# Kernel tuning notes

Measured on AMD Instinct MI355X. Metric: run time of the kernel, lower is better.

The kernel has to match this reference:

```python
import jax, jax.numpy as jnp
import numpy as np

N0, N1, N2 = 400000, 100000, 20000   # source nodes per sampled layer; dst nodes are a prefix
E1, E2 = 1000000, 200000
IN, HID, HEADS, OUT = 128, 256, 4, 47
C = HID // HEADS
EPS = 1e-5
NEG_SLOPE = 0.2


def setup_inputs() -> dict:
    key = jax.random.key(0)
    ks = jax.random.split(key, 20)
    def rn(i, shape, s=0.1):
        return jax.random.normal(ks[i], shape, jnp.float32) * s
    inp = {}
    inp["x"] = jax.random.normal(ks[0], (N0, IN), jnp.float32)
    inp["src1"] = jax.random.randint(ks[1], (E1,), 0, N0, jnp.int32)
    inp["dst1"] = jax.random.randint(ks[2], (E1,), 0, N1, jnp.int32)
    inp["src2"] = jax.random.randint(ks[3], (E2,), 0, N1, jnp.int32)
    inp["dst2"] = jax.random.randint(ks[4], (E2,), 0, N2, jnp.int32)
    # layer 1 GAT + skip + BN
    inp["W1"] = rn(5, (IN, HID)); inp["a_src1"] = rn(6, (HEADS, C)); inp["a_dst1"] = rn(7, (HEADS, C))
    inp["b1"] = jnp.zeros((HID,), jnp.float32)
    inp["Wsk1"] = rn(8, (IN, HID)); inp["bsk1"] = jnp.zeros((HID,), jnp.float32)
    inp["g1"] = jnp.ones((HID,), jnp.float32); inp["be1"] = jnp.zeros((HID,), jnp.float32)
    # layer 2 GAT + skip + BN
    inp["W2"] = rn(9, (HID, HID)); inp["a_src2"] = rn(10, (HEADS, C)); inp["a_dst2"] = rn(11, (HEADS, C))
    inp["b2"] = jnp.zeros((HID,), jnp.float32)
    inp["Wsk2"] = rn(12, (HID, HID)); inp["bsk2"] = jnp.zeros((HID,), jnp.float32)
    inp["g2"] = jnp.ones((HID,), jnp.float32); inp["be2"] = jnp.zeros((HID,), jnp.float32)
    # MLP head
    inp["Wm1"] = rn(13, (HID, HID)); inp["bm1"] = jnp.zeros((HID,), jnp.float32)
    inp["gm"] = jnp.ones((HID,), jnp.float32); inp["bem"] = jnp.zeros((HID,), jnp.float32)
    inp["Wm2"] = rn(14, (HID, OUT)); inp["bm2"] = jnp.zeros((OUT,), jnp.float32)
    return inp


def batch_norm(x, gamma, beta):
    mu = jnp.mean(x, axis=0)
    var = jnp.mean(jnp.square(x - mu), axis=0)  # biased var, as torch BN training
    return (x - mu) * jax.lax.rsqrt(var + EPS) * gamma + beta


def edge_softmax(logits, dst, n_dst):
    # logits: [E, H]; softmax over incoming edges per destination node
    m = jax.ops.segment_max(logits, dst, num_segments=n_dst)
    m = jax.lax.stop_gradient(jnp.where(jnp.isfinite(m), m, 0.0))
    e = jnp.exp(logits - m[dst])
    s = jax.ops.segment_sum(e, dst, num_segments=n_dst)
    return e / (s[dst] + 1e-16)


def gat_layer(x, n_dst, src, dst, W, a_src, a_dst, b, Wsk, bsk, gamma, beta):
    # GATConv (PyG, shared src/dst linear since in_channels is int) on bipartite (x, x[:n_dst])
    xp = (x @ W).reshape(-1, HEADS, C)                       # [N, H, C]
    al_s = jnp.einsum('nhc,hc->nh', xp, a_src)               # [N, H]
    al_d = jnp.einsum('nhc,hc->nh', xp[:n_dst], a_dst)       # [n_dst, H]
    logits = jax.nn.leaky_relu(al_s[src] + al_d[dst], NEG_SLOPE)   # [E, H]
    alpha = edge_softmax(logits, dst, n_dst)                 # [E, H]
    msg = xp[src] * alpha[:, :, None]                        # [E, H, C]
    out = jax.ops.segment_sum(msg, dst, num_segments=n_dst).reshape(n_dst, HID) + b
    out = out + x[:n_dst] @ Wsk + bsk                        # skip connection
    return jax.nn.elu(batch_norm(out, gamma, beta))          # dropout omitted (eval)


def reference(x, src1, dst1, src2, dst2,
              W1, a_src1, a_dst1, b1, Wsk1, bsk1, g1, be1,
              W2, a_src2, a_dst2, b2, Wsk2, bsk2, g2, be2,
              Wm1, bm1, gm, bem, Wm2, bm2):
    h = gat_layer(x, N1, src1, dst1, W1, a_src1, a_dst1, b1, Wsk1, bsk1, g1, be1)
    h = gat_layer(h, N2, src2, dst2, W2, a_src2, a_dst2, b2, Wsk2, bsk2, g2, be2)
    # MLP head: Linear -> BN -> ReLU -> (Dropout) -> Linear
    h = jax.nn.relu(batch_norm(h @ Wm1 + bm1, gm, bem))
    return h @ Wm2 + bm2                                     # logits [N2, OUT]
```

## Files before the change

kernel.cpp:

```cpp
#include <hip/hip_runtime.h>
#include <math.h>

constexpr int kN0 = 400000, kN1 = 100000, kN2 = 20000;
constexpr int kE1 = 1000000, kE2 = 200000;
constexpr int kIN = 128, kHID = 256, kOUT = 47;
constexpr float kEPS = 1e-5f, kNEG = 0.2f;

#define DEV static __device__ __forceinline__

typedef __attribute__((ext_vector_type(8))) short short8;
typedef __attribute__((ext_vector_type(4))) float f32x4;

DEV float b2f(unsigned short u) { return __uint_as_float(((unsigned)u) << 16); }
DEV unsigned short f2bf(float f) {
    unsigned u = __float_as_uint(f);
    unsigned r = (u + 0x7fffu + ((u >> 16) & 1u)) >> 16;
    return (unsigned short)r;
}
DEV float lrelu(float v) { return v > 0.f ? v : kNEG * v; }

DEV void gload_lds16(const void* g, void* l) {
    __builtin_amdgcn_global_load_lds(
        (const __attribute__((address_space(1))) void*)g,
        (__attribute__((address_space(3))) void*)l, 16, 0, 0);
}

constexpr int kNZreg = 1536 + 2 * kN1 + 2 * kN2;
__global__ void prep_all(const float* __restrict__ W1, const float* __restrict__ as1,
                         const float* __restrict__ ad1,
                         const float* __restrict__ W2, const float* __restrict__ as2,
                         const float* __restrict__ ad2,
                         const float* __restrict__ Wsk1, const float* __restrict__ Wsk2,
                         const float* __restrict__ Wm1,
                         float* __restrict__ zreg,
                         unsigned short* __restrict__ v1t, unsigned short* __restrict__ v2t,
                         unsigned short* __restrict__ Wcat1t,
                         unsigned short* __restrict__ Wcat2t,
                         unsigned short* __restrict__ Wm1t) {
    int i = blockIdx.x * blockDim.x + threadIdx.x;
    if (i < kNZreg) { zreg[i] = 0.f; return; }
    i -= kNZreg;
    if (i < 2048) {
        int j = i >> 7, k = i & 127;
        float s = 0.f;
        if (j < 8) {
            int h = j & 3;
            const float* a = (j >= 4) ? ad1 : as1;
            for (int c = 0; c < 64; ++c) s += W1[(size_t)k * 256 + h * 64 + c] * a[h * 64 + c];
        }
        v1t[i] = f2bf(s);
        return;
    }
    i -= 2048;
    if (i < 4096) {
        int j = i >> 8, k = i & 255;
        float s = 0.f;
        if (j < 8) {
            int h = j & 3;
            const float* a = (j >= 4) ? ad2 : as2;
            for (int c = 0; c < 64; ++c) s += W2[(size_t)k * 256 + h * 64 + c] * a[h * 64 + c];
        }
        v2t[i] = f2bf(s);
        return;
    }
    i -= 4096;
    if (i < 163840) {
        int n = i / 640, k = i % 640;
        float v;
        if (k < 512) { int h = k >> 7, kin = k & 127; v = ((n >> 6) == h) ? W1[(size_t)kin * 256 + n] : 0.f; }
        else v = Wsk1[(size_t)(k - 512) * 256 + n];
        Wcat1t[i] = f2bf(v);
        return;
    }
    i -= 163840;
    if (i < 327680) {
        int n = i / 1280, k = i % 1280;
        float v;
        if (k < 1024) { int h = k >> 8, kin = k & 255; v = ((n >> 6) == h) ? W2[(size_t)kin * 256 + n] : 0.f; }
        else v = Wsk2[(size_t)(k - 1024) * 256 + n];
        Wcat2t[i] = f2bf(v);
        return;
    }
    i -= 327680;
    if (i < 65536) {
        int n = i >> 8, k = i & 255;
        Wm1t[i] = f2bf(Wm1[(size_t)k * 256 + n]);
    }
}

__global__ __launch_bounds__(256) void conv_als_mfma(const float* __restrict__ x,
                                                     const unsigned short* __restrict__ v1t,
                                                     unsigned short* __restrict__ xb,
                                                     float* __restrict__ als,
                                                     float* __restrict__ ald) {
    int wid = threadIdx.x >> 6, lane = threadIdx.x & 63;
    int l15 = lane & 15, l4 = lane >> 4;
    short8 bfr[4];
    #pragma unroll
    for (int ks = 0; ks < 4; ++ks)
        bfr[ks] = *reinterpret_cast<const short8*>(&v1t[l15 * 128 + ks * 32 + l4 * 8]);

    const int ntile = kN0 / 16;
    int nw = gridDim.x * 4;
    for (int t = blockIdx.x * 4 + wid; t < ntile; t += nw) {
        int base = t * 16;
        int r = base + l15;
        f32x4 acc = (f32x4){0.f, 0.f, 0.f, 0.f};
        #pragma unroll
        for (int ks = 0; ks < 4; ++ks) {
            size_t o = (size_t)r * 128 + ks * 32 + l4 * 8;
            float4 xa = *reinterpret_cast<const float4*>(&x[o]);
            float4 xc = *reinterpret_cast<const float4*>(&x[o + 4]);
            short8 af;
            af[0] = (short)f2bf(xa.x); af[1] = (short)f2bf(xa.y);
            af[2] = (short)f2bf(xa.z); af[3] = (short)f2bf(xa.w);
            af[4] = (short)f2bf(xc.x); af[5] = (short)f2bf(xc.y);
            af[6] = (short)f2bf(xc.z); af[7] = (short)f2bf(xc.w);
            *reinterpret_cast<short8*>(&xb[o]) = af;
            acc = __builtin_amdgcn_mfma_f32_16x16x32_bf16(af, bfr[ks], acc, 0, 0, 0);
        }
        if (l15 < 8) {
            #pragma unroll
            for (int i = 0; i < 4; ++i) {
                int node = base + l4 * 4 + i;
                if (l15 < 4) als[(size_t)node * 4 + l15] = acc[i];
                else if (node < kN1) ald[(size_t)node * 4 + (l15 - 4)] = acc[i];
            }
        }
    }
}

template <bool AL>
__global__ __launch_bounds__(256) void bn_mfma(const unsigned short* __restrict__ X,
                                               const float* __restrict__ stats,
                                               const float* __restrict__ gamma,
                                               const float* __restrict__ beta,
                                               unsigned short* __restrict__ outb,
                                               const unsigned short* __restrict__ v2t,
                                               float* __restrict__ als,
                                               float* __restrict__ ald,
                                               int M, int Ndst) {
    __shared__ float smu[256], ssc[256], ssh[256];
    {
        int c = threadIdx.x;
        float invM = 1.f / (float)M;
        float mu = stats[c] * invM;
        float var = stats[256 + c] * invM - mu * mu;
        smu[c] = mu;
        ssc[c] = rsqrtf(var + kEPS) * gamma[c];
        ssh[c] = beta[c];
    }
    __syncthreads();

    int wid = threadIdx.x >> 6, lane = threadIdx.x & 63;
    int l15 = lane & 15, l4 = lane >> 4;
    short8 bfr[8];
    if (AL) {
        #pragma unroll
        for (int ks = 0; ks < 8; ++ks)
            bfr[ks] = *reinterpret_cast<const short8*>(&v2t[l15 * 256 + ks * 32 + l4 * 8]);
    }

    const int ntile = M / 16;
    int nw = gridDim.x * 4;
    for (int t = blockIdx.x * 4 + wid; t < ntile; t += nw) {
        int base = t * 16;
        int r = base + l15;
        f32x4 acc = (f32x4){0.f, 0.f, 0.f, 0.f};
        #pragma unroll
        for (int ks = 0; ks < 8; ++ks) {
            int c0 = ks * 32 + l4 * 8;
            size_t o = (size_t)r * 256 + c0;
            short8 xr = *reinterpret_cast<const short8*>(&X[o]);
            float4 mua = *reinterpret_cast<const float4*>(&smu[c0]);
            float4 muc = *reinterpret_cast<const float4*>(&smu[c0 + 4]);
            float4 sca = *reinterpret_cast<const float4*>(&ssc[c0]);
            float4 scc = *reinterpret_cast<const float4*>(&ssc[c0 + 4]);
            float4 sha = *reinterpret_cast<const float4*>(&ssh[c0]);
            float4 shc = *reinterpret_cast<const float4*>(&ssh[c0 + 4]);
            float v[8];
            v[0] = (b2f((unsigned short)xr[0]) - mua.x) * sca.x + sha.x;
            v[1] = (b2f((unsigned short)xr[1]) - mua.y) * sca.y + sha.y;
            v[2] = (b2f((unsigned short)xr[2]) - mua.z) * sca.z + sha.z;
            v[3] = (b2f((unsigned short)xr[3]) - mua.w) * sca.w + sha.w;
            v[4] = (b2f((unsigned short)xr[4]) - muc.x) * scc.x + shc.x;
            v[5] = (b2f((unsigned short)xr[5]) - muc.y) * scc.y + shc.y;
            v[6] = (b2f((unsigned short)xr[6]) - muc.z) * scc.z + shc.z;
            v[7] = (b2f((unsigned short)xr[7]) - muc.w) * scc.w + shc.w;
            short8 af;
            #pragma unroll
            for (int i = 0; i < 8; ++i) {
                float tv = v[i] > 0.f ? v[i] : expm1f(v[i]);
                af[i] = (short)f2bf(tv);
            }
            *reinterpret_cast<short8*>(&outb[o]) = af;
            if (AL) acc = __builtin_amdgcn_mfma_f32_16x16x32_bf16(af, bfr[ks], acc, 0, 0, 0);
        }
        if (AL && l15 < 8) {
            #pragma unroll
            for (int i = 0; i < 4; ++i) {
                int node = base + l4 * 4 + i;
                if (l15 < 4) als[(size_t)node * 4 + l15] = acc[i];
                else if (node < Ndst) ald[(size_t)node * 4 + (l15 - 4)] = acc[i];
            }
        }
    }
}

__global__ void hist_both(const int* __restrict__ dst1, int* __restrict__ cnt1, int E1,
                          const int* __restrict__ dst2, int* __restrict__ cnt2, int E2) {
    int e = blockIdx.x * blockDim.x + threadIdx.x;
    if (e < E1) atomicAdd(&cnt1[dst1[e]], 1);
    else if (e - E1 < E2) atomicAdd(&cnt2[dst2[e - E1]], 1);
}

__global__ __launch_bounds__(256) void scan_block_both(const int* __restrict__ cnt1, int n1,
                                                       int* __restrict__ offs1, int* __restrict__ bsum1, int nb1,
                                                       const int* __restrict__ cnt2, int n2,
                                                       int* __restrict__ offs2, int* __restrict__ bsum2) {
    const int* counts; int n; int* offs; int* bsum; int b;
    if ((int)blockIdx.x < nb1) { counts = cnt1; n = n1; offs = offs1; bsum = bsum1; b = blockIdx.x; }
    else { counts = cnt2; n = n2; offs = offs2; bsum = bsum2; b = blockIdx.x - nb1; }
    __shared__ int sh[256];
    int tid = threadIdx.x;
    int base = b * 1024 + tid * 4;
    int c0 = (base + 0 < n) ? counts[base + 0] : 0;
    int c1 = (base + 1 < n) ? counts[base + 1] : 0;
    int c2 = (base + 2 < n) ? counts[base + 2] : 0;
    int c3 = (base + 3 < n) ? counts[base + 3] : 0;
    int tot = c0 + c1 + c2 + c3;
    sh[tid] = tot;
    __syncthreads();
    for (int o = 1; o < 256; o <<= 1) {
        int t = (tid >= o) ? sh[tid - o] : 0;
        __syncthreads();
        sh[tid] += t;
        __syncthreads();
    }
    int excl = sh[tid] - tot;
    if (base + 0 < n) offs[base + 0] = excl;
    if (base + 1 < n) offs[base + 1] = excl + c0;
    if (base + 2 < n) offs[base + 2] = excl + c0 + c1;
    if (base + 3 < n) offs[base + 3] = excl + c0 + c1 + c2;
    if (tid == 255) bsum[b] = sh[255];
}

__global__ __launch_bounds__(256) void scan_bsums_both(const int* __restrict__ bsum1,
                                                       int* __restrict__ bscan1, int nb1,
                                                       const int* __restrict__ bsum2,
                                                       int* __restrict__ bscan2, int nb2) {
    __shared__ int sh[256];
    int tid = threadIdx.x;
    int v = (tid < nb1) ? bsum1[tid] : 0;
    sh[tid] = v;
    __syncthreads();
    for (int o = 1; o < 256; o <<= 1) {
        int t = (tid >= o) ? sh[tid - o] : 0;
        __syncthreads();
        sh[tid] += t;
        __syncthreads();
    }
    if (tid < nb1) bscan1[tid] = sh[tid] - v;
    __syncthreads();
    int v2 = (tid < nb2) ? bsum2[tid] : 0;
    sh[tid] = v2;
    __syncthreads();
    for (int o = 1; o < 256; o <<= 1) {
        int t = (tid >= o) ? sh[tid - o] : 0;
        __syncthreads();
        sh[tid] += t;
        __syncthreads();
    }
    if (tid < nb2) bscan2[tid] = sh[tid] - v2;
}

__global__ void scan_add_both(int* __restrict__ offs1, const int* __restrict__ bscan1,
                              const int* __restrict__ cnt1, int n1,
                              int* __restrict__ offs2, const int* __restrict__ bscan2,
                              const int* __restrict__ cnt2, int n2) {
    int i = blockIdx.x * blockDim.x + threadIdx.x;
    if (i < n1) {
        int v = offs1[i] + bscan1[i >> 10];
        offs1[i] = v;
        if (i == n1 - 1) offs1[n1] = v + cnt1[i];
    } else {
        int j = i - n1;
        if (j < n2) {
            int v = offs2[j] + bscan2[j >> 10];
            offs2[j] = v;
            if (j == n2 - 1) offs2[n2] = v + cnt2[j];
        }
    }
}

__global__ void csr_scatter_w(const int* __restrict__ dst, const int* __restrict__ src,
                              const int* __restrict__ offs,
                              const float* __restrict__ als, const float* __restrict__ ald,
                              int* __restrict__ cur, int* __restrict__ srcs,
                              float4* __restrict__ wbuf, int E) {
    int e = blockIdx.x * blockDim.x + threadIdx.x;
    if (e >= E) return;
    int d = dst[e], s = src[e];
    int pos = offs[d] + atomicAdd(&cur[d], 1);
    srcs[pos] = s;
    float4 a = *reinterpret_cast<const float4*>(&als[(size_t)s * 4]);
    float4 b = *reinterpret_cast<const float4*>(&ald[(size_t)d * 4]);
    float4 w;
    w.x = expf(lrelu(a.x + b.x));
    w.y = expf(lrelu(a.y + b.y));
    w.z = expf(lrelu(a.z + b.z));
    w.w = expf(lrelu(a.w + b.w));
    wbuf[pos] = w;
}

template <bool OUTBF, bool STATS>
__global__ __launch_bounds__(512) void gemm_pipe(const unsigned short* __restrict__ A1, int K1,
                                                 const unsigned short* __restrict__ A2, int K2,
                                                 const unsigned short* __restrict__ Bt,
                                                 void* __restrict__ Cv,
                                                 const float* __restrict__ bias1,
                                                 const float* __restrict__ bias2,
                                                 float* __restrict__ stats,
                                                 int M, int N, int rs, int kwin) {
    __shared__ unsigned short SH[4][128 * 64];
    const int tid = threadIdx.x;
    const int wid = tid >> 6, lane = tid & 63;
    const int wr = wid >> 2, wc = wid & 3;
    const int l15 = lane & 15, l4 = lane >> 4;
    const int m0 = blockIdx.y * 128, n0 = blockIdx.x * 128;
    const int rsub = lane >> 3;
    const int kslot = (lane & 7) ^ rsub;
    const int KB = K1 + K2;
    const int nwin = kwin >> 6;
    const int nt = nwin + (K2 >> 6);
    const int wbase = n0 * rs;

    auto stage = [&](int buf, int t) {
        const unsigned short* Asrc; int ka, lda, gk;
        if (t < nwin) { gk = wbase + (t << 6); Asrc = A1; ka = gk; lda = K1; }
        else { int t2 = t - nwin; gk = K1 + (t2 << 6); Asrc = A2; ka = t2 << 6; lda = K2; }
        #pragma unroll
        for (int c = 0; c < 2; ++c) {
            int q = wid * 2 + c;
            int rowA = m0 + q * 8 + rsub; if (rowA > M - 1) rowA = M - 1;
            gload_lds16(Asrc + (size_t)rowA * lda + ka + kslot * 8, &SH[buf][q * 512]);
            int rowB = n0 + q * 8 + rsub;
            gload_lds16(Bt + (size_t)rowB * KB + gk + kslot * 8, &SH[2 + buf][q * 512]);
        }
    };

    f32x4 acc[4][2];
    #pragma unroll
    for (int i = 0; i < 4; ++i)
        #pragma unroll
        for (int j = 0; j < 2; ++j) acc[i][j] = (f32x4){0.f, 0.f, 0.f, 0.f};

    stage(0, 0);
    __syncthreads();
    for (int t = 0; t < nt; ++t) {
        if (t + 1 < nt) stage((t + 1) & 1, t + 1);
        int b = t & 1;
        short8 af[2][4], bf[2][2];
        #pragma unroll
        for (int kk = 0; kk < 2; ++kk) {
            #pragma unroll
            for (int mi = 0; mi < 4; ++mi) {
                int row = wr * 64 + mi * 16 + l15;
                af[kk][mi] = *reinterpret_cast<const short8*>(
                    &SH[b][row * 64 + (((kk * 4 + l4) ^ (row & 7)) << 3)]);
            }
            #pragma unroll
            for (int ni = 0; ni < 2; ++ni) {
                int row = wc * 32 + ni * 16 + l15;
                bf[kk][ni] = *reinterpret_cast<const short8*>(
                    &SH[2 + b][row * 64 + (((kk * 4 + l4) ^ (row & 7)) << 3)]);
            }
        }
        #pragma unroll
        for (int kk = 0; kk < 2; ++kk)
            #pragma unroll
            for (int mi = 0; mi < 4; ++mi)
                #pragma unroll
                for (int ni = 0; ni < 2; ++ni)
                    acc[mi][ni] = __builtin_amdgcn_mfma_f32_16x16x32_bf16(
                        af[kk][mi], bf[kk][ni], acc[mi][ni], 0, 0, 0);
        __syncthreads();
    }

    float csum[2] = {0.f, 0.f}, csq[2] = {0.f, 0.f};
    unsigned short* LB = (unsigned short*)SH;
    float* LF = (float*)SH;
    #pragma unroll
    for (int mi = 0; mi < 4; ++mi) {
        int lrow0 = wr * 64 + mi * 16 + l4 * 4;
        #pragma unroll
        for (int ni = 0; ni < 2; ++ni) {
            int lcol = wc * 32 + ni * 16 + l15;
            int col = n0 + lcol;
            float badd = 0.f;
            if (bias1) badd += bias1[col];
            if (bias2) badd += bias2[col];
            f32x4 v = acc[mi][ni];
            #pragma unroll
            for (int i = 0; i < 4; ++i) {
                float o = v[i] + badd;
                if (STATS && (m0 + lrow0 + i) < M) { csum[ni] += o; csq[ni] += o * o; }
                if (OUTBF) LB[(lrow0 + i) * 128 + lcol] = f2bf(o);
                else LF[(lrow0 + i) * 128 + lcol] = o;
            }
        }
    }
    if (STATS) {
        #pragma unroll
        for (int ni = 0; ni < 2; ++ni) {
            float s = csum[ni], q = csq[ni];
            s += __shfl_xor(s, 16, 64); q += __shfl_xor(q, 16, 64);
            s += __shfl_xor(s, 32, 64); q += __shfl_xor(q, 32, 64);
            if (l4 == 0) {
                int col = n0 + wc * 32 + ni * 16 + l15;
                atomicAdd(&stats[col], s);
                atomicAdd(&stats[256 + col], q);
            }
        }
    }
    __syncthreads();
    if (OUTBF) {
        unsigned short* Cb = (unsigned short*)Cv;
        #pragma unroll
        for (int it = 0; it < 4; ++it) {
            int lin = (it * 512 + tid) * 8;
            int r = lin >> 7, c0 = lin & 127;
            int gr = m0 + r;
            if (gr < M)
                *reinterpret_cast<short8*>(&Cb[(size_t)gr * N + n0 + c0]) =
                    *reinterpret_cast<const short8*>(&LB[lin]);
        }
    } else {
        float* Cf = (float*)Cv;
        #pragma unroll
        for (int it = 0; it < 8; ++it) {
            int lin = (it * 512 + tid) * 4;
            int r = lin >> 7, c0 = lin & 127;
            int gr = m0 + r;
            if (gr < M)
                *reinterpret_cast<float4*>(&Cf[(size_t)gr * N + n0 + c0]) =
                    *reinterpret_cast<const float4*>(&LF[lin]);
        }
    }
}

__global__ __launch_bounds__(256) void fused_agg1(const unsigned short* __restrict__ xb,
                                                  const float4* __restrict__ wbuf,
                                                  const int* __restrict__ srcs,
                                                  const int* __restrict__ offs,
                                                  unsigned short* __restrict__ Agg, int Ndst) {
    int d = blockIdx.x * 4 + (threadIdx.x >> 6);
    if (d >= Ndst) return;
    int lane = threadIdx.x & 63;
    int beg = offs[d], end = offs[d + 1];
    float ac[4][2] = {};
    float se0 = 0.f, se1 = 0.f, se2 = 0.f, se3 = 0.f;

    auto edge = [&](int i) {
        int s = srcs[i];
        float4 w = wbuf[i];
        unsigned xv = *reinterpret_cast<const unsigned*>(&xb[(size_t)s * 128 + lane * 2]);
        se0 += w.x; se1 += w.y; se2 += w.z; se3 += w.w;
        float fx = b2f((unsigned short)(xv & 0xffff));
        float fy = b2f((unsigned short)(xv >> 16));
        ac[0][0] = fmaf(w.x, fx, ac[0][0]); ac[0][1] = fmaf(w.x, fy, ac[0][1]);
        ac[1][0] = fmaf(w.y, fx, ac[1][0]); ac[1][1] = fmaf(w.y, fy, ac[1][1]);
        ac[2][0] = fmaf(w.z, fx, ac[2][0]); ac[2][1] = fmaf(w.z, fy, ac[2][1]);
        ac[3][0] = fmaf(w.w, fx, ac[3][0]); ac[3][1] = fmaf(w.w, fy, ac[3][1]);
    };
    int i = beg;
    for (; i + 4 <= end; i += 4) { edge(i); edge(i + 1); edge(i + 2); edge(i + 3); }
    for (; i < end; ++i) edge(i);

    float inv0 = 1.f / (se0 + 1e-16f), inv1 = 1.f / (se1 + 1e-16f);
    float inv2 = 1.f / (se2 + 1e-16f), inv3 = 1.f / (se3 + 1e-16f);
    unsigned short* row = Agg + (size_t)d * 512;
    ushort2 o;
    o.x = f2bf(ac[0][0] * inv0); o.y = f2bf(ac[0][1] * inv0);
    *reinterpret_cast<ushort2*>(&row[0 * 128 + lane * 2]) = o;
    o.x = f2bf(ac[1][0] * inv1); o.y = f2bf(ac[1][1] * inv1);
    *reinterpret_cast<ushort2*>(&row[1 * 128 + lane * 2]) = o;
    o.x = f2bf(ac[2][0] * inv2); o.y = f2bf(ac[2][1] * inv2);
    *reinterpret_cast<ushort2*>(&row[2 * 128 + lane * 2]) = o;
    o.x = f2bf(ac[3][0] * inv3); o.y = f2bf(ac[3][1] * inv3);
    *reinterpret_cast<ushort2*>(&row[3 * 128 + lane * 2]) = o;
}

__global__ __launch_bounds__(256) void fused_agg2(const unsigned short* __restrict__ hb,
                                                  const float4* __restrict__ wbuf,
                                                  const int* __restrict__ srcs,
                                                  const int* __restrict__ offs,
                                                  unsigned short* __restrict__ Agg, int Ndst) {
    int d = blockIdx.x * 4 + (threadIdx.x >> 6);
    if (d >= Ndst) return;
    int lane = threadIdx.x & 63;
    int beg = offs[d], end = offs[d + 1];
    float ac[4][4] = {};
    float se0 = 0.f, se1 = 0.f, se2 = 0.f, se3 = 0.f;

    auto edge = [&](int i) {
        int s = srcs[i];
        float4 w = wbuf[i];
        ushort4 xv = *reinterpret_cast<const ushort4*>(&hb[(size_t)s * 256 + lane * 4]);
        se0 += w.x; se1 += w.y; se2 += w.z; se3 += w.w;
        float f0 = b2f(xv.x), f1 = b2f(xv.y), f2 = b2f(xv.z), f3 = b2f(xv.w);
        ac[0][0] = fmaf(w.x, f0, ac[0][0]); ac[0][1] = fmaf(w.x, f1, ac[0][1]);
        ac[0][2] = fmaf(w.x, f2, ac[0][2]); ac[0][3] = fmaf(w.x, f3, ac[0][3]);
        ac[1][0] = fmaf(w.y, f0, ac[1][0]); ac[1][1] = fmaf(w.y, f1, ac[1][1]);
        ac[1][2] = fmaf(w.y, f2, ac[1][2]); ac[1][3] = fmaf(w.y, f3, ac[1][3]);
        ac[2][0] = fmaf(w.z, f0, ac[2][0]); ac[2][1] = fmaf(w.z, f1, ac[2][1]);
        ac[2][2] = fmaf(w.z, f2, ac[2][2]); ac[2][3] = fmaf(w.z, f3, ac[2][3]);
        ac[3][0] = fmaf(w.w, f0, ac[3][0]); ac[3][1] = fmaf(w.w, f1, ac[3][1]);
        ac[3][2] = fmaf(w.w, f2, ac[3][2]); ac[3][3] = fmaf(w.w, f3, ac[3][3]);
    };
    int i = beg;
    for (; i + 2 <= end; i += 2) { edge(i); edge(i + 1); }
    for (; i < end; ++i) edge(i);

    float inv[4] = {1.f / (se0 + 1e-16f), 1.f / (se1 + 1e-16f),
                    1.f / (se2 + 1e-16f), 1.f / (se3 + 1e-16f)};
    unsigned short* row = Agg + (size_t)d * 1024;
    #pragma unroll
    for (int h = 0; h < 4; ++h) {
        ushort4 o;
        o.x = f2bf(ac[h][0] * inv[h]); o.y = f2bf(ac[h][1] * inv[h]);
        o.z = f2bf(ac[h][2] * inv[h]); o.w = f2bf(ac[h][3] * inv[h]);
        *reinterpret_cast<ushort4*>(&row[h * 256 + lane * 4]) = o;
    }
}

__global__ __launch_bounds__(256) void gemm64_bn(const unsigned short* __restrict__ A,
                                                 const float* __restrict__ B,
                                                 float* __restrict__ Cmat,
                                                 const float* __restrict__ bias,
                                                 const float* __restrict__ stats,
                                                 const float* __restrict__ gamma,
                                                 const float* __restrict__ beta,
                                                 int M, int N, int K) {
    __shared__ float As[32][68];
    __shared__ float Bs[32][68];
    __shared__ float bnsc[256], bnsh[256];
    const int tid = threadIdx.x;
    {
        int c = tid;
        float invM = 1.f / (float)M;
        float mu = stats[c] * invM;
        float var = stats[256 + c] * invM - mu * mu;
        float sc = rsqrtf(var + kEPS) * gamma[c];
        bnsc[c] = sc;
        bnsh[c] = beta[c] - mu * sc;
    }
    __syncthreads();
    const int tx = tid & 15, ty = tid >> 4;
    const int m0 = blockIdx.y * 64, n0 = blockIdx.x * 64;
    float acc[4][4] = {};

    for (int k0 = 0; k0 < K; k0 += 32) {
        #pragma unroll
        for (int t = 0; t < 2; ++t) {
            int i = tid + t * 256;
            int row = i >> 3;
            int kq = (i & 7) << 2;
            ushort4 u = make_ushort4(0, 0, 0, 0);
            int gr = m0 + row;
            if (gr < M) u = *reinterpret_cast<const ushort4*>(&A[(size_t)gr * K + k0 + kq]);
            #pragma unroll
            for (int j = 0; j < 4; ++j) {
                int k = k0 + kq + j;
                unsigned short uv = (j == 0) ? u.x : (j == 1) ? u.y : (j == 2) ? u.z : u.w;
                float v = b2f(uv) * bnsc[k] + bnsh[k];
                As[kq + j][row] = fmaxf(v, 0.f);
            }
        }
        #pragma unroll
        for (int t = 0; t < 2; ++t) {
            int i = tid + t * 256;
            int kr = i >> 4;
            int cq = (i & 15) << 2;
            #pragma unroll
            for (int j = 0; j < 4; ++j) {
                int gc = n0 + cq + j;
                Bs[kr][cq + j] = (gc < N) ? B[(size_t)(k0 + kr) * N + gc] : 0.f;
            }
        }
        __syncthreads();
        #pragma unroll
        for (int kk = 0; kk < 32; ++kk) {
            float4 a4 = *reinterpret_cast<const float4*>(&As[kk][ty << 2]);
            float4 b4 = *reinterpret_cast<const float4*>(&Bs[kk][tx << 2]);
            float a[4] = {a4.x, a4.y, a4.z, a4.w};
            float b[4] = {b4.x, b4.y, b4.z, b4.w};
            #pragma unroll
            for (int i2 = 0; i2 < 4; ++i2)
                #pragma unroll
                for (int j = 0; j < 4; ++j)
                    acc[i2][j] = fmaf(a[i2], b[j], acc[i2][j]);
        }
        __syncthreads();
    }

    #pragma unroll
    for (int i2 = 0; i2 < 4; ++i2) {
        int row = m0 + (ty << 2) + i2;
        if (row >= M) continue;
        #pragma unroll
        for (int j = 0; j < 4; ++j) {
            int col = n0 + (tx << 2) + j;
            if (col >= N) continue;
            Cmat[(size_t)row * N + col] = acc[i2][j] + bias[col];
        }
    }
}

extern "C" void kernel_launch(void* const* d_in, const int* in_sizes, int n_in,
                              void* d_out, int out_size, void* d_ws, size_t ws_size,
                              hipStream_t stream) {
    (void)in_sizes; (void)n_in; (void)out_size; (void)ws_size;

    const float* x      = (const float*)d_in[0];
    const int*   src1   = (const int*)d_in[1];
    const int*   dst1   = (const int*)d_in[2];
    const int*   src2   = (const int*)d_in[3];
    const int*   dst2   = (const int*)d_in[4];
    const float* W1     = (const float*)d_in[5];
    const float* a_src1 = (const float*)d_in[6];
    const float* a_dst1 = (const float*)d_in[7];
    const float* b1     = (const float*)d_in[8];
    const float* Wsk1   = (const float*)d_in[9];
    const float* bsk1   = (const float*)d_in[10];
    const float* g1     = (const float*)d_in[11];
    const float* be1    = (const float*)d_in[12];
    const float* W2     = (const float*)d_in[13];
    const float* a_src2 = (const float*)d_in[14];
    const float* a_dst2 = (const float*)d_in[15];
    const float* b2     = (const float*)d_in[16];
    const float* Wsk2   = (const float*)d_in[17];
    const float* bsk2   = (const float*)d_in[18];
    const float* g2     = (const float*)d_in[19];
    const float* be2    = (const float*)d_in[20];
    const float* Wm1    = (const float*)d_in[21];
    const float* bm1    = (const float*)d_in[22];
    const float* gm     = (const float*)d_in[23];
    const float* bem    = (const float*)d_in[24];
    const float* Wm2    = (const float*)d_in[25];
    const float* bm2    = (const float*)d_in[26];

    float* ws = (float*)d_ws;
    size_t off = 0;
    auto alloc = [&](size_t n) { float* p = ws + off; off += n; return p; };
    unsigned short* xb    = (unsigned short*)alloc((size_t)kN0 * 128 / 2);
    unsigned short* Agg1  = (unsigned short*)alloc((size_t)kN1 * 512 / 2);
    unsigned short* Agg2  = (unsigned short*)alloc((size_t)kN2 * 1024 / 2);
    unsigned short* h1pre = (unsigned short*)alloc((size_t)kN1 * 256 / 2);
    unsigned short* h1b   = (unsigned short*)alloc((size_t)kN1 * 256 / 2);
    unsigned short* h2pre = (unsigned short*)alloc((size_t)kN2 * 256 / 2);
    unsigned short* h2b   = (unsigned short*)alloc((size_t)kN2 * 256 / 2);
    unsigned short* h3pre = (unsigned short*)alloc((size_t)kN2 * 256 / 2);
    unsigned short* Wcat1t = (unsigned short*)alloc(256 * 640 / 2);
    unsigned short* Wcat2t = (unsigned short*)alloc(256 * 1280 / 2);
    unsigned short* Wm1t   = (unsigned short*)alloc(256 * 256 / 2);
    unsigned short* v1t    = (unsigned short*)alloc(16 * 128 / 2);
    unsigned short* v2t    = (unsigned short*)alloc(16 * 256 / 2);
    float4* w1buf = (float4*)alloc((size_t)kE1 * 4);
    float4* w2buf = (float4*)alloc((size_t)kE2 * 4);
    float* als1 = alloc((size_t)kN0 * 4);
    float* ald1 = alloc((size_t)kN1 * 4);
    float* als2 = alloc((size_t)kN1 * 4);
    float* ald2 = alloc((size_t)kN2 * 4);
    float* zreg = alloc(kNZreg);
    float* stats1 = zreg, *stats2 = zreg + 512, *stats3 = zreg + 1024;
    int* cnt1 = (int*)(zreg + 1536);
    int* cur1 = cnt1 + kN1;
    int* cnt2 = cur1 + kN1;
    int* cur2 = cnt2 + kN2;
    int* srcs1  = (int*)alloc(kE1);
    int* offs1  = (int*)alloc(kN1 + 4);
    int* bsum1  = (int*)alloc(128);
    int* bscan1 = (int*)alloc(128);
    int* srcs2  = (int*)alloc(kE2);
    int* offs2  = (int*)alloc(kN2 + 4);
    int* bsum2  = (int*)alloc(128);
    int* bscan2 = (int*)alloc(128);

    hipStream_t st = stream;
    const int nb1 = (kN1 + 1023) / 1024;
    const int nb2 = (kN2 + 1023) / 1024;

    prep_all<<<(kNZreg + 563200 + 255) / 256, 256, 0, st>>>(
        W1, a_src1, a_dst1, W2, a_src2, a_dst2, Wsk1, Wsk2, Wm1,
        zreg, v1t, v2t, Wcat1t, Wcat2t, Wm1t);

    conv_als_mfma<<<2048, 256, 0, st>>>(x, v1t, xb, als1, ald1);

    hist_both<<<(kE1 + kE2 + 255) / 256, 256, 0, st>>>(dst1, cnt1, kE1, dst2, cnt2, kE2);
    scan_block_both<<<nb1 + nb2, 256, 0, st>>>(cnt1, kN1, offs1, bsum1, nb1, cnt2, kN2, offs2, bsum2);
    scan_bsums_both<<<1, 256, 0, st>>>(bsum1, bscan1, nb1, bsum2, bscan2, nb2);
    scan_add_both<<<(kN1 + kN2 + 255) / 256, 256, 0, st>>>(offs1, bscan1, cnt1, kN1,
                                                           offs2, bscan2, cnt2, kN2);
    csr_scatter_w<<<(kE1 + 255) / 256, 256, 0, st>>>(dst1, src1, offs1, als1, ald1,
                                                     cur1, srcs1, w1buf, kE1);

    fused_agg1<<<(kN1 + 3) / 4, 256, 0, st>>>(xb, w1buf, srcs1, offs1, Agg1, kN1);
    gemm_pipe<true, true><<<dim3(2, (kN1 + 127) / 128), 512, 0, st>>>(
        Agg1, 512, xb, 128, Wcat1t, h1pre, b1, bsk1, stats1, kN1, 256, 2, 256);
    bn_mfma<true><<<1024, 256, 0, st>>>(h1pre, stats1, g1, be1, h1b, v2t, als2, ald2, kN1, kN2);

    csr_scatter_w<<<(kE2 + 255) / 256, 256, 0, st>>>(dst2, src2, offs2, als2, ald2,
                                                     cur2, srcs2, w2buf, kE2);
    fused_agg2<<<(kN2 + 3) / 4, 256, 0, st>>>(h1b, w2buf, srcs2, offs2, Agg2, kN2);
    gemm_pipe<true, true><<<dim3(2, (kN2 + 127) / 128), 512, 0, st>>>(
        Agg2, 1024, h1b, 256, Wcat2t, h2pre, b2, bsk2, stats2, kN2, 256, 4, 512);
    bn_mfma<false><<<1024, 256, 0, st>>>(h2pre, stats2, g2, be2, h2b, nullptr, nullptr, nullptr,
                                         kN2, 0);

    gemm_pipe<true, true><<<dim3(2, (kN2 + 127) / 128), 512, 0, st>>>(
        h2b, 256, nullptr, 0, Wm1t, h3pre, bm1, nullptr, stats3, kN2, 256, 0, 256);
    gemm64_bn<<<dim3(1, (kN2 + 63) / 64), 256, 0, st>>>(
        h3pre, Wm2, (float*)d_out, bm2, stats3, gm, bem, kN2, kOUT, 256);
}
```

Measured before the change: 542.2 us.

## Fuse histogram into conv kernel, merge scan passes, batch aggregation loads

Measured after the change: 522.6 us. -3.6%, faster.

```diff
diff --git a/kernel.cpp b/kernel.cpp
--- a/kernel.cpp
+++ b/kernel.cpp
@@ -88,11 +88,22 @@
     }
 }
 
-__global__ __launch_bounds__(256) void conv_als_mfma(const float* __restrict__ x,
+constexpr int kConvBlocks = 2048;
+__global__ __launch_bounds__(256) void conv_als_hist(const float* __restrict__ x,
                                                      const unsigned short* __restrict__ v1t,
                                                      unsigned short* __restrict__ xb,
                                                      float* __restrict__ als,
-                                                     float* __restrict__ ald) {
+                                                     float* __restrict__ ald,
+                                                     const int* __restrict__ dst1,
+                                                     int* __restrict__ cnt1,
+                                                     const int* __restrict__ dst2,
+                                                     int* __restrict__ cnt2) {
+    if ((int)blockIdx.x >= kConvBlocks) {
+        int e = ((int)blockIdx.x - kConvBlocks) * 256 + threadIdx.x;
+        if (e < kE1) atomicAdd(&cnt1[dst1[e]], 1);
+        else { e -= kE1; if (e < kE2) atomicAdd(&cnt2[dst2[e]], 1); }
+        return;
+    }
     int wid = threadIdx.x >> 6, lane = threadIdx.x & 63;
     int l15 = lane & 15, l4 = lane >> 4;
     short8 bfr[4];
@@ -101,7 +112,7 @@
         bfr[ks] = *reinterpret_cast<const short8*>(&v1t[l15 * 128 + ks * 32 + l4 * 8]);
 
     const int ntile = kN0 / 16;
-    int nw = gridDim.x * 4;
+    const int nw = kConvBlocks * 4;
     for (int t = blockIdx.x * 4 + wid; t < ntile; t += nw) {
         int base = t * 16;
         int r = base + l15;
@@ -205,13 +216,6 @@
             }
         }
     }
-}
-
-__global__ void hist_both(const int* __restrict__ dst1, int* __restrict__ cnt1, int E1,
-                          const int* __restrict__ dst2, int* __restrict__ cnt2, int E2) {
-    int e = blockIdx.x * blockDim.x + threadIdx.x;
-    if (e < E1) atomicAdd(&cnt1[dst1[e]], 1);
-    else if (e - E1 < E2) atomicAdd(&cnt2[dst2[e - E1]], 1);
 }
 
 __global__ __launch_bounds__(256) void scan_block_both(const int* __restrict__ cnt1, int n1,
@@ -245,48 +249,29 @@
     if (tid == 255) bsum[b] = sh[255];
 }
 
-__global__ __launch_bounds__(256) void scan_bsums_both(const int* __restrict__ bsum1,
-                                                       int* __restrict__ bscan1, int nb1,
-                                                       const int* __restrict__ bsum2,
-                                                       int* __restrict__ bscan2, int nb2) {
-    __shared__ int sh[256];
-    int tid = threadIdx.x;
-    int v = (tid < nb1) ? bsum1[tid] : 0;
-    sh[tid] = v;
+__global__ __launch_bounds__(256) void scan_add_both(int* __restrict__ offs1,
+                                                     const int* __restrict__ bsum1,
+                                                     const int* __restrict__ cnt1, int n1, int nb1,
+                                                     int* __restrict__ offs2,
+                                                     const int* __restrict__ bsum2,
+                                                     const int* __restrict__ cnt2, int n2, int nb2) {
+    __shared__ int sb1[128], sb2[32];
+    if (threadIdx.x == 0) {
+        int acc = 0;
+        for (int j = 0; j < nb1; ++j) { sb1[j] = acc; acc += bsum1[j]; }
+        acc = 0;
+        for (int j = 0; j < nb2; ++j) { sb2[j] = acc; acc += bsum2[j]; }
+    }
     __syncthreads();
-    for (int o = 1; o < 256; o <<= 1) {
-        int t = (tid >= o) ? sh[tid - o] : 0;
-        __syncthreads();
-        sh[tid] += t;
-        __syncthreads();
-    }
-    if (tid < nb1) bscan1[tid] = sh[tid] - v;
-    __syncthreads();
-    int v2 = (tid < nb2) ? bsum2[tid] : 0;
-    sh[tid] = v2;
-    __syncthreads();
-    for (int o = 1; o < 256; o <<= 1) {
-        int t = (tid >= o) ? sh[tid - o] : 0;
-        __syncthreads();
-        sh[tid] += t;
-        __syncthreads();
-    }
-    if (tid < nb2) bscan2[tid] = sh[tid] - v2;
-}
-
-__global__ void scan_add_both(int* __restrict__ offs1, const int* __restrict__ bscan1,
-                              const int* __restrict__ cnt1, int n1,
-                              int* __restrict__ offs2, const int* __restrict__ bscan2,
-                              const int* __restrict__ cnt2, int n2) {
     int i = blockIdx.x * blockDim.x + threadIdx.x;
     if (i < n1) {
-        int v = offs1[i] + bscan1[i >> 10];
+        int v = offs1[i] + sb1[i >> 10];
         offs1[i] = v;
         if (i == n1 - 1) offs1[n1] = v + cnt1[i];
     } else {
         int j = i - n1;
         if (j < n2) {
-            int v = offs2[j] + bscan2[j >> 10];
+            int v = offs2[j] + sb2[j >> 10];
             offs2[j] = v;
             if (j == n2 - 1) offs2[n2] = v + cnt2[j];
         }
@@ -461,21 +446,29 @@
     float ac[4][2] = {};
     float se0 = 0.f, se1 = 0.f, se2 = 0.f, se3 = 0.f;
 
-    auto edge = [&](int i) {
-        int s = srcs[i];
-        float4 w = wbuf[i];
-        unsigned xv = *reinterpret_cast<const unsigned*>(&xb[(size_t)s * 128 + lane * 2]);
-        se0 += w.x; se1 += w.y; se2 += w.z; se3 += w.w;
-        float fx = b2f((unsigned short)(xv & 0xffff));
-        float fy = b2f((unsigned short)(xv >> 16));
-        ac[0][0] = fmaf(w.x, fx, ac[0][0]); ac[0][1] = fmaf(w.x, fy, ac[0][1]);
-        ac[1][0] = fmaf(w.y, fx, ac[1][0]); ac[1][1] = fmaf(w.y, fy, ac[1][1]);
-        ac[2][0] = fmaf(w.z, fx, ac[2][0]); ac[2][1] = fmaf(w.z, fy, ac[2][1]);
-        ac[3][0] = fmaf(w.w, fx, ac[3][0]); ac[3][1] = fmaf(w.w, fy, ac[3][1]);
-    };
-    int i = beg;
-    for (; i + 4 <= end; i += 4) { edge(i); edge(i + 1); edge(i + 2); edge(i + 3); }
-    for (; i < end; ++i) edge(i);
+    for (int i = beg; i < end; i += 4) {
+        int s[4]; float4 w[4]; unsigned xv[4];
+        #pragma unroll
+        for (int j = 0; j < 4; ++j) {
+            int idx = i + j < end ? i + j : end - 1;
+            s[j] = srcs[idx];
+            if (i + j < end) w[j] = wbuf[idx];
+            else w[j] = make_float4(0.f, 0.f, 0.f, 0.f);
+        }
+        #pragma unroll
+        for (int j = 0; j < 4; ++j)
+            xv[j] = *reinterpret_cast<const unsigned*>(&xb[(size_t)s[j] * 128 + lane * 2]);
+        #pragma unroll
+        for (int j = 0; j < 4; ++j) {
+            se0 += w[j].x; se1 += w[j].y; se2 += w[j].z; se3 += w[j].w;
+            float fx = b2f((unsigned short)(xv[j] & 0xffff));
+            float fy = b2f((unsigned short)(xv[j] >> 16));
+            ac[0][0] = fmaf(w[j].x, fx, ac[0][0]); ac[0][1] = fmaf(w[j].x, fy, ac[0][1]);
+            ac[1][0] = fmaf(w[j].y, fx, ac[1][0]); ac[1][1] = fmaf(w[j].y, fy, ac[1][1]);
+            ac[2][0] = fmaf(w[j].z, fx, ac[2][0]); ac[2][1] = fmaf(w[j].z, fy, ac[2][1]);
+            ac[3][0] = fmaf(w[j].w, fx, ac[3][0]); ac[3][1] = fmaf(w[j].w, fy, ac[3][1]);
+        }
+    }
 
     float inv0 = 1.f / (se0 + 1e-16f), inv1 = 1.f / (se1 + 1e-16f);
     float inv2 = 1.f / (se2 + 1e-16f), inv3 = 1.f / (se3 + 1e-16f);
@@ -503,24 +496,32 @@
     float ac[4][4] = {};
     float se0 = 0.f, se1 = 0.f, se2 = 0.f, se3 = 0.f;
 
-    auto edge = [&](int i) {
-        int s = srcs[i];
-        float4 w = wbuf[i];
-        ushort4 xv = *reinterpret_cast<const ushort4*>(&hb[(size_t)s * 256 + lane * 4]);
-        se0 += w.x; se1 += w.y; se2 += w.z; se3 += w.w;
-        float f0 = b2f(xv.x), f1 = b2f(xv.y), f2 = b2f(xv.z), f3 = b2f(xv.w);
-        ac[0][0] = fmaf(w.x, f0, ac[0][0]); ac[0][1] = fmaf(w.x, f1, ac[0][1]);
-        ac[0][2] = fmaf(w.x, f2, ac[0][2]); ac[0][3] = fmaf(w.x, f3, ac[0][3]);
-        ac[1][0] = fmaf(w.y, f0, ac[1][0]); ac[1][1] = fmaf(w.y, f1, ac[1][1]);
-        ac[1][2] = fmaf(w.y, f2, ac[1][2]); ac[1][3] = fmaf(w.y, f3, ac[1][3]);
-        ac[2][0] = fmaf(w.z, f0, ac[2][0]); ac[2][1] = fmaf(w.z, f1, ac[2][1]);
-        ac[2][2] = fmaf(w.z, f2, ac[2][2]); ac[2][3] = fmaf(w.z, f3, ac[2][3]);
-        ac[3][0] = fmaf(w.w, f0, ac[3][0]); ac[3][1] = fmaf(w.w, f1, ac[3][1]);
-        ac[3][2] = fmaf(w.w, f2, ac[3][2]); ac[3][3] = fmaf(w.w, f3, ac[3][3]);
-    };
-    int i = beg;
-    for (; i + 2 <= end; i += 2) { edge(i); edge(i + 1); }
-    for (; i < end; ++i) edge(i);
+    for (int i = beg; i < end; i += 4) {
+        int s[4]; float4 w[4]; ushort4 xv[4];
+        #pragma unroll
+        for (int j = 0; j < 4; ++j) {
+            int idx = i + j < end ? i + j : end - 1;
+            s[j] = srcs[idx];
+            if (i + j < end) w[j] = wbuf[idx];
+            else w[j] = make_float4(0.f, 0.f, 0.f, 0.f);
+        }
+        #pragma unroll
+        for (int j = 0; j < 4; ++j)
+            xv[j] = *reinterpret_cast<const ushort4*>(&hb[(size_t)s[j] * 256 + lane * 4]);
+        #pragma unroll
+        for (int j = 0; j < 4; ++j) {
+            se0 += w[j].x; se1 += w[j].y; se2 += w[j].z; se3 += w[j].w;
+            float f0 = b2f(xv[j].x), f1 = b2f(xv[j].y), f2 = b2f(xv[j].z), f3 = b2f(xv[j].w);
+            ac[0][0] = fmaf(w[j].x, f0, ac[0][0]); ac[0][1] = fmaf(w[j].x, f1, ac[0][1]);
+            ac[0][2] = fmaf(w[j].x, f2, ac[0][2]); ac[0][3] = fmaf(w[j].x, f3, ac[0][3]);
+            ac[1][0] = fmaf(w[j].y, f0, ac[1][0]); ac[1][1] = fmaf(w[j].y, f1, ac[1][1]);
+            ac[1][2] = fmaf(w[j].y, f2, ac[1][2]); ac[1][3] = fmaf(w[j].y, f3, ac[1][3]);
+            ac[2][0] = fmaf(w[j].z, f0, ac[2][0]); ac[2][1] = fmaf(w[j].z, f1, ac[2][1]);
+            ac[2][2] = fmaf(w[j].z, f2, ac[2][2]); ac[2][3] = fmaf(w[j].z, f3, ac[2][3]);
+            ac[3][0] = fmaf(w[j].w, f0, ac[3][0]); ac[3][1] = fmaf(w[j].w, f1, ac[3][1]);
+            ac[3][2] = fmaf(w[j].w, f2, ac[3][2]); ac[3][3] = fmaf(w[j].w, f3, ac[3][3]);
+        }
+    }
 
     float inv[4] = {1.f / (se0 + 1e-16f), 1.f / (se1 + 1e-16f),
                     1.f / (se2 + 1e-16f), 1.f / (se3 + 1e-16f)};
@@ -681,11 +682,9 @@
     int* srcs1  = (int*)alloc(kE1);
     int* offs1  = (int*)alloc(kN1 + 4);
     int* bsum1  = (int*)alloc(128);
-    int* bscan1 = (int*)alloc(128);
     int* srcs2  = (int*)alloc(kE2);
     int* offs2  = (int*)alloc(kN2 + 4);
     int* bsum2  = (int*)alloc(128);
-    int* bscan2 = (int*)alloc(128);
 
     hipStream_t st = stream;
     const int nb1 = (kN1 + 1023) / 1024;
@@ -695,13 +694,13 @@
         W1, a_src1, a_dst1, W2, a_src2, a_dst2, Wsk1, Wsk2, Wm1,
         zreg, v1t, v2t, Wcat1t, Wcat2t, Wm1t);
 
-    conv_als_mfma<<<2048, 256, 0, st>>>(x, v1t, xb, als1, ald1);
-
-    hist_both<<<(kE1 + kE2 + 255) / 256, 256, 0, st>>>(dst1, cnt1, kE1, dst2, cnt2, kE2);
+    const int histBlocks = (kE1 + kE2 + 255) / 256;
+    conv_als_hist<<<kConvBlocks + histBlocks, 256, 0, st>>>(
+        x, v1t, xb, als1, ald1, dst1, cnt1, dst2, cnt2);
+
     scan_block_both<<<nb1 + nb2, 256, 0, st>>>(cnt1, kN1, offs1, bsum1, nb1, cnt2, kN2, offs2, bsum2);
-    scan_bsums_both<<<1, 256, 0, st>>>(bsum1, bscan1, nb1, bsum2, bscan2, nb2);
-    scan_add_both<<<(kN1 + kN2 + 255) / 256, 256, 0, st>>>(offs1, bscan1, cnt1, kN1,
-                                                           offs2, bscan2, cnt2, kN2);
+    scan_add_both<<<(kN1 + kN2 + 255) / 256, 256, 0, st>>>(offs1, bsum1, cnt1, kN1, nb1,
+                                                           offs2, bsum2, cnt2, kN2, nb2);
     csr_scatter_w<<<(kE1 + 255) / 256, 256, 0, st>>>(dst1, src1, offs1, als1, ald1,
                                                      cur1, srcs1, w1buf, kE1);
 
```
